# Kernel optimization log

Measured on AMD Instinct MI355X. Metric: run time of the kernel, lower is better.

## Reference

```python
import jax, jax.numpy as jnp
import numpy as np

B, S, E = 8, 2048, 768
U = 1024          # cfc_units (total NCP units; motor neurons = first E)
BB = 512          # CfC backbone width
H_MLP = 4 * E

def _lecun_tanh(x):
    return 1.7159 * jnp.tanh(0.666 * x)

def _layernorm(x, g, b, eps=1e-5):
    mu = jnp.mean(x, axis=-1, keepdims=True)
    var = jnp.var(x, axis=-1, keepdims=True)
    return (x - mu) * jax.lax.rsqrt(var + eps) * g + b


def setup_inputs() -> dict:
    key = jax.random.key(0)
    ks = jax.random.split(key, 16)
    sc = 0.02
    d = {}
    d["x"] = jax.random.normal(ks[0], (B, S, E), dtype=jnp.float32)
    d["hx"] = jnp.zeros((B, U), dtype=jnp.float32)
    # ln_1 / ln_2
    d["ln1_g"] = jnp.ones((E,), jnp.float32); d["ln1_b"] = jnp.zeros((E,), jnp.float32)
    d["ln2_g"] = jnp.ones((E,), jnp.float32); d["ln2_b"] = jnp.zeros((E,), jnp.float32)
    # CfC cell (default mode): backbone over concat([input, h]) then ff1/ff2/time_a/time_b heads
    d["W_bb"] = sc * jax.random.normal(ks[1], (E + U, BB), jnp.float32)
    d["b_bb"] = jnp.zeros((BB,), jnp.float32)
    d["W_ff1"] = sc * jax.random.normal(ks[2], (BB, U), jnp.float32)
    d["b_ff1"] = jnp.zeros((U,), jnp.float32)
    d["W_ff2"] = sc * jax.random.normal(ks[3], (BB, U), jnp.float32)
    d["b_ff2"] = jnp.zeros((U,), jnp.float32)
    d["W_ta"] = sc * jax.random.normal(ks[4], (BB, U), jnp.float32)
    d["b_ta"] = jnp.zeros((U,), jnp.float32)
    d["W_tb"] = sc * jax.random.normal(ks[5], (BB, U), jnp.float32)
    d["b_tb"] = jnp.zeros((U,), jnp.float32)
    # LIF gate params (per n_embd unit)
    d["lif_thr"] = jnp.full((E,), 0.01, jnp.float32)
    d["lif_leak"] = jnp.full((E,), 2.0, jnp.float32)
    d["lif_steep"] = jnp.full((E,), 2.0, jnp.float32)
    # MLP
    d["W1"] = sc * jax.random.normal(ks[6], (E, H_MLP), jnp.float32)
    d["b1"] = jnp.zeros((H_MLP,), jnp.float32)
    d["W2"] = sc * jax.random.normal(ks[7], (H_MLP, E), jnp.float32)
    d["b2"] = jnp.zeros((E,), jnp.float32)
    return d


def _cfc_scan(normed, hx, W_bb, b_bb, W_ff1, b_ff1, W_ff2, b_ff2, W_ta, b_ta, W_tb, b_tb):
    # normed: [B, S, E]; hx: [B, U]. Closed-form continuous-time cell, ts=1.
    xs = jnp.swapaxes(normed, 0, 1)  # [S, B, E]

    def step(h, x_t):
        cat = jnp.concatenate([x_t, h], axis=-1)           # [B, E+U]
        bb = _lecun_tanh(cat @ W_bb + b_bb)                # [B, BB]
        ff1 = _lecun_tanh(bb @ W_ff1 + b_ff1)              # [B, U]
        ff2 = _lecun_tanh(bb @ W_ff2 + b_ff2)
        t_interp = jax.nn.sigmoid((bb @ W_ta + b_ta) + (bb @ W_tb + b_tb))
        h_new = ff1 * (1.0 - t_interp) + t_interp * ff2    # [B, U]
        return h_new, h_new[:, :E]                         # motor neurons -> output

    new_hx, ys = jax.lax.scan(step, hx, xs)
    return jnp.swapaxes(ys, 0, 1), new_hx                  # [B, S, E], [B, U]


def _lif_gate(x, thr, leak, steep):
    threshold = jnp.abs(thr) * 0.1
    leak_s = jax.nn.sigmoid(leak)
    steepness = jax.nn.softplus(steep)
    potential = jnp.abs(x)
    fire = jax.nn.sigmoid(steepness * (potential - threshold))
    gate = fire + leak_s * (1.0 - fire)
    return x * gate


def reference(x, hx, ln1_g, ln1_b, ln2_g, ln2_b,
              W_bb, b_bb, W_ff1, b_ff1, W_ff2, b_ff2, W_ta, b_ta, W_tb, b_tb,
              lif_thr, lif_leak, lif_steep, W1, b1, W2, b2):
    normed = _layernorm(x, ln1_g, ln1_b)
    cfc_out, new_hx = _cfc_scan(normed, hx, W_bb, b_bb, W_ff1, b_ff1,
                                W_ff2, b_ff2, W_ta, b_ta, W_tb, b_tb)
    cfc_out = _lif_gate(cfc_out, lif_thr, lif_leak, lif_steep)
    x = x + cfc_out  # dropout = identity in eval
    h2 = _layernorm(x, ln2_g, ln2_b)
    mlp = jax.nn.gelu(h2 @ W1 + b1, approximate=False) @ W2 + b2
    x = x + mlp
    return x, new_hx
```

## Files before the change

kernel.cpp:

```cpp
#include <hip/hip_runtime.h>
#include <math.h>

#define NB 8
#define NS 2048
#define NE 768
#define NU 1024
#define NBB 512
#define NH 3072
#define NBS (NB*NS)
#define NWG 128

typedef float f32x4v __attribute__((ext_vector_type(4)));
typedef __bf16 bf16x8v __attribute__((ext_vector_type(8)));
typedef unsigned short u16x8v __attribute__((ext_vector_type(8)));
typedef unsigned short u16x4v __attribute__((ext_vector_type(4)));

__device__ __forceinline__ unsigned short f2bf(float f) {
  unsigned int u = __builtin_bit_cast(unsigned int, f);
  u = (u + 0x7fffu + ((u >> 16) & 1u)) >> 16;
  return (unsigned short)u;
}
__device__ __forceinline__ float bf2f(unsigned short h) {
  unsigned int u = ((unsigned int)h) << 16;
  return __builtin_bit_cast(float, u);
}

__device__ __forceinline__ float ald(const float* p) {
  return __hip_atomic_load((const float*)p, __ATOMIC_RELAXED, __HIP_MEMORY_SCOPE_AGENT);
}
__device__ __forceinline__ void ast(float* p, float v) {
  __hip_atomic_store(p, v, __ATOMIC_RELAXED, __HIP_MEMORY_SCOPE_AGENT);
}
__device__ __forceinline__ float2 ald2(const float* p) {
  unsigned long long v = __hip_atomic_load((const unsigned long long*)p,
                             __ATOMIC_RELAXED, __HIP_MEMORY_SCOPE_AGENT);
  return __builtin_bit_cast(float2, v);
}
__device__ __forceinline__ unsigned aldu(const unsigned* p) {
  return __hip_atomic_load(p, __ATOMIC_RELAXED, __HIP_MEMORY_SCOPE_AGENT);
}
__device__ __forceinline__ void astu(unsigned* p, unsigned v) {
  __hip_atomic_store(p, v, __ATOMIC_RELAXED, __HIP_MEMORY_SCOPE_AGENT);
}

__device__ __forceinline__ void gbar4(unsigned* bar, int bx, unsigned tick) {
  __syncthreads();
  int tid = threadIdx.x;
  unsigned* flag = &bar[768];
  if (bx == 0) {
    if (tid < 64) {
      if (tid == 0) astu(&bar[0], tick);
      unsigned m;
      do {
        unsigned a = aldu(&bar[tid * 4]);
        unsigned b = aldu(&bar[(tid + 64) * 4]);
        m = a < b ? a : b;
        #pragma unroll
        for (int s = 1; s < 64; s <<= 1) {
          unsigned o = __shfl_xor(m, s);
          m = m < o ? m : o;
        }
        if (m < tick) __builtin_amdgcn_s_sleep(1);
      } while (m < tick);
      if (tid == 0) astu(flag, tick);
    }
  } else {
    if (tid == 0) {
      astu(&bar[bx * 4], tick);
      while (aldu(flag) < tick) __builtin_amdgcn_s_sleep(1);
    }
  }
  __syncthreads();
}

__global__ __launch_bounds__(256) void tr_f32(const float* __restrict__ in,
                                              float* __restrict__ out, int R, int C) {
  __shared__ float tile[32][33];
  int c0 = blockIdx.x * 32, r0 = blockIdx.y * 32;
  int tx = threadIdx.x, ty = threadIdx.y;
  #pragma unroll
  for (int i = 0; i < 32; i += 8)
    tile[ty + i][tx] = in[(long)(r0 + ty + i) * C + c0 + tx];
  __syncthreads();
  #pragma unroll
  for (int i = 0; i < 32; i += 8)
    out[(long)(c0 + ty + i) * R + r0 + tx] = tile[tx][ty + i];
}

__global__ __launch_bounds__(256) void tr_f32_bf16(const float* __restrict__ in,
                                                   unsigned short* __restrict__ out, int R, int C) {
  __shared__ float tile[32][33];
  int c0 = blockIdx.x * 32, r0 = blockIdx.y * 32;
  int tx = threadIdx.x, ty = threadIdx.y;
  #pragma unroll
  for (int i = 0; i < 32; i += 8)
    tile[ty + i][tx] = in[(long)(r0 + ty + i) * C + c0 + tx];
  __syncthreads();
  #pragma unroll
  for (int i = 0; i < 32; i += 8)
    out[(long)(c0 + ty + i) * R + r0 + tx] = f2bf(tile[tx][ty + i]);
}

__global__ __launch_bounds__(256) void tr_f32_bf16split(const float* __restrict__ in,
    unsigned short* __restrict__ oh, unsigned short* __restrict__ ol, int R, int C) {
  __shared__ float tile[32][33];
  int c0 = blockIdx.x * 32, r0 = blockIdx.y * 32;
  int tx = threadIdx.x, ty = threadIdx.y;
  #pragma unroll
  for (int i = 0; i < 32; i += 8)
    tile[ty + i][tx] = in[(long)(r0 + ty + i) * C + c0 + tx];
  __syncthreads();
  #pragma unroll
  for (int i = 0; i < 32; i += 8) {
    float v = tile[tx][ty + i];
    unsigned short h = f2bf(v);
    long idx = (long)(c0 + ty + i) * R + r0 + tx;
    oh[idx] = h;
    ol[idx] = f2bf(v - bf2f(h));
  }
}

__global__ __launch_bounds__(256) void ln_kernel(const float* __restrict__ in,
    const float* __restrict__ gw, const float* __restrict__ bw,
    unsigned short* __restrict__ outh, unsigned short* __restrict__ outl) {
  int lane = threadIdx.x & 63;
  long row = (long)blockIdx.x * 4 + (threadIdx.x >> 6);
  const float4* rp = (const float4*)(in + row * NE);
  float4 v[3];
  float s = 0.f, sq = 0.f;
  #pragma unroll
  for (int j = 0; j < 3; ++j) {
    v[j] = rp[lane + j * 64];
    s += v[j].x + v[j].y + v[j].z + v[j].w;
    sq += v[j].x*v[j].x + v[j].y*v[j].y + v[j].z*v[j].z + v[j].w*v[j].w;
  }
  #pragma unroll
  for (int m = 1; m < 64; m <<= 1) { s += __shfl_xor(s, m); sq += __shfl_xor(sq, m); }
  float mu = s * (1.f / NE);
  float rs = rsqrtf(sq * (1.f / NE) - mu * mu + 1e-5f);
  #pragma unroll
  for (int j = 0; j < 3; ++j) {
    int c4 = lane + j * 64;
    float4 g4 = ((const float4*)gw)[c4];
    float4 b4 = ((const float4*)bw)[c4];
    float f0 = (v[j].x - mu) * rs * g4.x + b4.x;
    float f1 = (v[j].y - mu) * rs * g4.y + b4.y;
    float f2 = (v[j].z - mu) * rs * g4.z + b4.z;
    float f3 = (v[j].w - mu) * rs * g4.w + b4.w;
    u16x4v oh, ol;
    oh[0] = f2bf(f0); ol[0] = f2bf(f0 - bf2f(oh[0]));
    oh[1] = f2bf(f1); ol[1] = f2bf(f1 - bf2f(oh[1]));
    oh[2] = f2bf(f2); ol[2] = f2bf(f2 - bf2f(oh[2]));
    oh[3] = f2bf(f3); ol[3] = f2bf(f3 - bf2f(oh[3]));
    *(u16x4v*)(outh + row * NE + (long)c4 * 4) = oh;
    *(u16x4v*)(outl + row * NE + (long)c4 * 4) = ol;
  }
}

template<int EPI>
__global__ __launch_bounds__(256) void gemm_bf16(
    const unsigned short* __restrict__ A, const unsigned short* __restrict__ Bt,
    const float* __restrict__ bias, const float* res,
    float* Cf, unsigned short* Cb, int M, int N, int K)
{
  __shared__ unsigned short lA[128][72];
  __shared__ unsigned short lB[128][72];
  int tid = threadIdx.x;
  int lane = tid & 63, wave = tid >> 6;
  int wr = wave >> 1, wc = wave & 1;
  int r15 = lane & 15, hi = lane >> 4;
  int ntn = N >> 7;
  long m0 = (long)(blockIdx.x / ntn) << 7;
  long n0 = (long)(blockIdx.x % ntn) << 7;
  f32x4v acc[4][4];
  #pragma unroll
  for (int m = 0; m < 4; ++m)
    #pragma unroll
    for (int n = 0; n < 4; ++n) acc[m][n] = (f32x4v){0.f, 0.f, 0.f, 0.f};

  for (int kt = 0; kt < K; kt += 64) {
    u16x8v ra[4], rb[4];
    #pragma unroll
    for (int i = 0; i < 4; ++i) {
      int c = tid + (i << 8);
      int rw = c >> 3, ko = (c & 7) << 3;
      ra[i] = *(const u16x8v*)(A + (m0 + rw) * K + kt + ko);
      rb[i] = *(const u16x8v*)(Bt + (n0 + rw) * K + kt + ko);
    }
    __syncthreads();
    #pragma unroll
    for (int i = 0; i < 4; ++i) {
      int c = tid + (i << 8);
      int rw = c >> 3, ko = (c & 7) << 3;
      *(u16x8v*)(&lA[rw][ko]) = ra[i];
      *(u16x8v*)(&lB[rw][ko]) = rb[i];
    }
    __syncthreads();
    #pragma unroll
    for (int ks = 0; ks < 64; ks += 32) {
      bf16x8v af[4], bfr[4];
      #pragma unroll
      for (int m = 0; m < 4; ++m)
        af[m] = *(const bf16x8v*)(&lA[wr * 64 + m * 16 + r15][ks + hi * 8]);
      #pragma unroll
      for (int n = 0; n < 4; ++n)
        bfr[n] = *(const bf16x8v*)(&lB[wc * 64 + n * 16 + r15][ks + hi * 8]);
      #pragma unroll
      for (int m = 0; m < 4; ++m)
        #pragma unroll
        for (int n = 0; n < 4; ++n)
          acc[m][n] = __builtin_amdgcn_mfma_f32_16x16x32_bf16(af[m], bfr[n], acc[m][n], 0, 0, 0);
    }
  }
  #pragma unroll
  for (int m = 0; m < 4; ++m) {
    long rbase = m0 + wr * 64 + m * 16 + hi * 4;
    #pragma unroll
    for (int n = 0; n < 4; ++n) {
      long cg = n0 + wc * 64 + n * 16 + r15;
      float bs = (EPI == 3) ? 0.f : bias[cg];
      #pragma unroll
      for (int e = 0; e < 4; ++e) {
        long row = rbase + e;
        float vv = acc[m][n][e] + bs;
        if (EPI == 0) {
          Cf[row * N + cg] = vv;
        } else if (EPI == 1) {
          float gl = 0.5f * vv * (1.f + erff(vv * 0.70710678118f));
          Cb[row * N + cg] = f2bf(gl);
        } else if (EPI == 2) {
          Cf[row * N + cg] = vv + res[row * N + cg];
        } else {
          Cf[row * N + cg] += vv;
        }
      }
    }
  }
}

__global__ __launch_bounds__(256) void scan_kernel(
    const float* __restrict__ pre, const float* __restrict__ WhhT,
    const float* __restrict__ WhT,
    const float* __restrict__ bf1, const float* __restrict__ bf2,
    const float* __restrict__ bta, const float* __restrict__ btb,
    const float* __restrict__ hx,
    float* hbuf, float* bbf, float* __restrict__ cfc, unsigned* bar)
{
  __shared__ float lsd[NB * NU];
  __shared__ float lpart[4][4][2][8];
  int tid = threadIdx.x;
  int lane = tid & 63, wave = tid >> 6;
  int bx = blockIdx.x;
  int j1 = (bx << 2) + wave;
  int head = lane >> 4, v2 = (lane >> 3) & 1, jsub = lane & 7;
  int vg = (bx << 3) + (wave << 1) + v2;
  const float4* W14 = (const float4*)(WhhT + (long)j1 * NU);
  const float4* W24 = (const float4*)(WhT + ((long)head * NU + vg) * NBB);
  const float4* ls4 = (const float4*)lsd;
  float2* ls2 = (float2*)lsd;
  unsigned tick = 0;

  float4 wreg[4];
  #pragma unroll
  for (int c = 0; c < 4; ++c) wreg[c] = W14[(c << 6) + lane];
  float4 w2reg[16];
  #pragma unroll
  for (int c = 0; c < 16; ++c) w2reg[c] = W24[(c << 3) + jsub];

  int vl = tid >> 3, bq = tid & 7;
  int wv = vl >> 1, qq = vl & 1;
  int vo = (bx << 3) + vl;
  float cb1 = 0.f, cb2 = 0.f, cbt = 0.f;
  if (tid < 64) { cb1 = bf1[vo]; cb2 = bf2[vo]; cbt = bta[vo] + btb[vo]; }

  if (tid < 64) ast(&hbuf[(bx << 6) + tid], hx[(bx << 6) + tid]);

  float prv[8];
  if (lane == 0) {
    #pragma unroll
    for (int b = 0; b < 8; ++b) prv[b] = pre[((long)b * NS) * NBB + j1];
  }
  gbar4(bar, bx, ++tick);

  for (int t = 0; t < NS; ++t) {
    {
      float2 rv[16];
      #pragma unroll
      for (int i = 0; i < 16; ++i) rv[i] = ald2(&hbuf[(((i << 8) + tid) << 1)]);
      #pragma unroll
      for (int i = 0; i < 16; ++i) ls2[(i << 8) + tid] = rv[i];
    }
    __syncthreads();

    float a1[8];
    #pragma unroll
    for (int b = 0; b < 8; ++b) a1[b] = 0.f;
    #pragma unroll
    for (int c = 0; c < 4; ++c) {
      int idx = (c << 6) + lane;
      float4 w = wreg[c];
      #pragma unroll
      for (int b = 0; b < 8; ++b) {
        float4 hv = ls4[(b << 8) + idx];
        a1[b] += w.x * hv.x + w.y * hv.y + w.z * hv.z + w.w * hv.w;
      }
    }
    #pragma unroll
    for (int m = 1; m < 64; m <<= 1)
      #pragma unroll
      for (int b = 0; b < 8; ++b) a1[b] += __shfl_xor(a1[b], m);
    if (lane == 0) {
      #pragma unroll
      for (int b = 0; b < 8; ++b) {
        float s = a1[b] + prv[b];
        ast(&bbf[b * NBB + j1], 1.7159f * tanhf(0.666f * s));
      }
    }
    gbar4(bar, bx, ++tick);

    {
      float2 rv[8];
      #pragma unroll
      for (int i = 0; i < 8; ++i) rv[i] = ald2(&bbf[(((i << 8) + tid) << 1)]);
      #pragma unroll
      for (int i = 0; i < 8; ++i) ls2[(i << 8) + tid] = rv[i];
    }
    __syncthreads();

    float a2[8];
    #pragma unroll
    for (int b = 0; b < 8; ++b) a2[b] = 0.f;
    #pragma unroll
    for (int c = 0; c < 16; ++c) {
      int idx = (c << 3) + jsub;
      float4 w = w2reg[c];
      #pragma unroll
      for (int b = 0; b < 8; ++b) {
        float4 bv = ls4[(b << 7) + idx];
        a2[b] += w.x * bv.x + w.y * bv.y + w.z * bv.z + w.w * bv.w;
      }
    }
    #pragma unroll
    for (int m = 1; m < 8; m <<= 1)
      #pragma unroll
      for (int b = 0; b < 8; ++b) a2[b] += __shfl_xor(a2[b], m);
    if (jsub == 0) {
      #pragma unroll
      for (int b = 0; b < 8; ++b) lpart[wave][head][v2][b] = a2[b];
    }
    __syncthreads();
    if (tid < 64) {
      float d1 = lpart[wv][0][qq][bq] + cb1;
      float d2 = lpart[wv][1][qq][bq] + cb2;
      float dt = lpart[wv][2][qq][bq] + lpart[wv][3][qq][bq] + cbt;
      float f1 = 1.7159f * tanhf(0.666f * d1);
      float f2 = 1.7159f * tanhf(0.666f * d2);
      float ti = 1.f / (1.f + expf(-dt));
      float hn = f1 * (1.f - ti) + ti * f2;
      ast(&hbuf[bq * NU + vo], hn);
      if (vo < NE) cfc[((long)bq * NS + t) * NE + vo] = hn;
    }
    if (lane == 0 && t + 1 < NS) {
      #pragma unroll
      for (int b = 0; b < 8; ++b) prv[b] = pre[((long)b * NS + t + 1) * NBB + j1];
    }
    gbar4(bar, bx, ++tick);
  }
}

__global__ __launch_bounds__(256) void lif_kernel(
    const float* __restrict__ x, const float* __restrict__ cfc,
    const float* __restrict__ thr, const float* __restrict__ leak,
    const float* __restrict__ steep, const float* __restrict__ hbuf,
    float* __restrict__ x1, float* __restrict__ outTail)
{
  long i4 = (long)blockIdx.x * blockDim.x + threadIdx.x;
  float4 xv = ((const float4*)x)[i4];
  float4 cv = ((const float4*)cfc)[i4];
  int col = (int)((i4 << 2) % NE);
  float4 tv = *(const float4*)(thr + col);
  float4 lv = *(const float4*)(leak + col);
  float4 sv = *(const float4*)(steep + col);
  float4 r;
#define LIF1(comp) { \
    float th = fabsf(tv.comp) * 0.1f; \
    float ls = 1.f / (1.f + expf(-lv.comp)); \
    float sp = (sv.comp > 20.f) ? sv.comp : log1pf(expf(sv.comp)); \
    float fire = 1.f / (1.f + expf(-sp * (fabsf(cv.comp) - th))); \
    float gate = fire + ls * (1.f - fire); \
    r.comp = xv.comp + cv.comp * gate; }
  LIF1(x) LIF1(y) LIF1(z) LIF1(w)
#undef LIF1
  ((float4*)x1)[i4] = r;
  if (i4 < (NB * NU / 4)) {
    const float* hp = hbuf + (i4 << 2);
    float4 hv; hv.x = ald(hp); hv.y = ald(hp + 1); hv.z = ald(hp + 2); hv.w = ald(hp + 3);
    ((float4*)outTail)[i4] = hv;
  }
}

extern "C" void kernel_launch(void* const* d_in, const int* in_sizes, int n_in,
                              void* d_out, int out_size, void* d_ws, size_t ws_size,
                              hipStream_t stream) {
  (void)in_sizes; (void)n_in; (void)out_size; (void)ws_size;
  const float* x     = (const float*)d_in[0];
  const float* hx    = (const float*)d_in[1];
  const float* ln1g  = (const float*)d_in[2];
  const float* ln1b  = (const float*)d_in[3];
  const float* ln2g  = (const float*)d_in[4];
  const float* ln2b  = (const float*)d_in[5];
  const float* Wbb   = (const float*)d_in[6];
  const float* bbb   = (const float*)d_in[7];
  const float* Wff1  = (const float*)d_in[8];
  const float* bff1  = (const float*)d_in[9];
  const float* Wff2  = (const float*)d_in[10];
  const float* bff2  = (const float*)d_in[11];
  const float* Wta   = (const float*)d_in[12];
  const float* btaP  = (const float*)d_in[13];
  const float* Wtb   = (const float*)d_in[14];
  const float* btbP  = (const float*)d_in[15];
  const float* lthr  = (const float*)d_in[16];
  const float* lleak = (const float*)d_in[17];
  const float* lstp  = (const float*)d_in[18];
  const float* W1    = (const float*)d_in[19];
  const float* b1    = (const float*)d_in[20];
  const float* W2    = (const float*)d_in[21];
  const float* b2    = (const float*)d_in[22];

  char* base = (char*)d_ws;
  unsigned short* normedH = (unsigned short*)base;
  float* pre   = (float*)(base + 25165824);
  float* cfc   = (float*)(base + 58720256);
  unsigned short* gelu = (unsigned short*)base;
  unsigned short* normedL = (unsigned short*)(base + 109051904);
  unsigned short* h2      = (unsigned short*)(base + 109051904);
  unsigned short* wtbbH = (unsigned short*)(base + 134217728);
  float* whhT  = (float*)(base + 135004160);
  float* whT   = (float*)(base + 137101312);
  unsigned short* w1t = (unsigned short*)(base + 145489920);
  unsigned short* w2t = (unsigned short*)(base + 150208512);
  float* hbuf  = (float*)(base + 154927104);
  float* bbf   = (float*)(base + 154959872);
  unsigned* bar = (unsigned*)(base + 154976256);
  unsigned short* wtbbL = (unsigned short*)(base + 154980352);
  float* xout  = (float*)d_out;
  float* outTail = xout + (size_t)NBS * NE;
  unsigned short* lnlo_dummy = (unsigned short*)base;

  dim3 b328(32, 8);
  tr_f32_bf16split<<<dim3(512/32, 768/32), b328, 0, stream>>>(Wbb, wtbbH, wtbbL, 768, 512);
  tr_f32<<<dim3(512/32, 1024/32), b328, 0, stream>>>(Wbb + 768*512, whhT, 1024, 512);
  tr_f32<<<dim3(1024/32, 512/32), b328, 0, stream>>>(Wff1, whT + 0*(size_t)NU*NBB, 512, 1024);
  tr_f32<<<dim3(1024/32, 512/32), b328, 0, stream>>>(Wff2, whT + 1*(size_t)NU*NBB, 512, 1024);
  tr_f32<<<dim3(1024/32, 512/32), b328, 0, stream>>>(Wta,  whT + 2*(size_t)NU*NBB, 512, 1024);
  tr_f32<<<dim3(1024/32, 512/32), b328, 0, stream>>>(Wtb,  whT + 3*(size_t)NU*NBB, 512, 1024);
  tr_f32_bf16<<<dim3(3072/32, 768/32), b328, 0, stream>>>(W1, w1t, 768, 3072);
  tr_f32_bf16<<<dim3(768/32, 3072/32), b328, 0, stream>>>(W2, w2t, 3072, 768);

  ln_kernel<<<NBS/4, 256, 0, stream>>>(x, ln1g, ln1b, normedH, normedL);
  gemm_bf16<0><<<(NBS/128)*(NBB/128), 256, 0, stream>>>(normedH, wtbbH, bbb, nullptr,
                                                        pre, nullptr, NBS, NBB, NE);
  gemm_bf16<3><<<(NBS/128)*(NBB/128), 256, 0, stream>>>(normedH, wtbbL, bbb, nullptr,
                                                        pre, nullptr, NBS, NBB, NE);
  gemm_bf16<3><<<(NBS/128)*(NBB/128), 256, 0, stream>>>(normedL, wtbbH, bbb, nullptr,
                                                        pre, nullptr, NBS, NBB, NE);

  hipMemsetAsync(bar, 0, 4096, stream);

  scan_kernel<<<NWG, 256, 0, stream>>>(pre, whhT, whT, bff1, bff2, btaP, btbP, hx,
                                       hbuf, bbf, cfc, bar);

  lif_kernel<<<(NBS*NE/4)/256, 256, 0, stream>>>(x, cfc, lthr, lleak, lstp, hbuf, xout, outTail);
  ln_kernel<<<NBS/4, 256, 0, stream>>>(xout, ln2g, ln2b, h2, lnlo_dummy);
  gemm_bf16<1><<<(NBS/128)*(NH/128), 256, 0, stream>>>(h2, w1t, b1, nullptr,
                                                       nullptr, gelu, NBS, NH, NE);
  gemm_bf16<2><<<(NBS/128)*(NE/128), 256, 0, stream>>>(gelu, w2t, b2, xout,
                                                       xout, nullptr, NBS, NE, NH);
}
```

Measured before the change: 21.56 ms.

## Redesign scan grid barrier with per-block release flags and batched pre loads

The grid barrier now pads arrival slots to 64 bytes and gives each block its own release flag, which block 0 writes directly. The s_sleep backoff is removed so waiters spin tightly. The per-step global load of the precomputed backbone input is replaced by loading 64 timesteps into LDS at once, and the cfc output store is moved after the barrier so it is off the critical path. Together these aim to shorten the sequential scan's per-step latency. The cost is heavier spinning traffic and the barrier buffer moving to a new workspace region.

```diff
diff --git a/kernel.cpp b/kernel.cpp
--- a/kernel.cpp
+++ b/kernel.cpp
@@ -43,31 +43,30 @@
   __hip_atomic_store(p, v, __ATOMIC_RELAXED, __HIP_MEMORY_SCOPE_AGENT);
 }
 
-__device__ __forceinline__ void gbar4(unsigned* bar, int bx, unsigned tick) {
+__device__ __forceinline__ void gbar5(unsigned* bar, int bx, unsigned tick) {
   __syncthreads();
   int tid = threadIdx.x;
-  unsigned* flag = &bar[768];
   if (bx == 0) {
     if (tid < 64) {
       if (tid == 0) astu(&bar[0], tick);
       unsigned m;
       do {
-        unsigned a = aldu(&bar[tid * 4]);
-        unsigned b = aldu(&bar[(tid + 64) * 4]);
+        unsigned a = aldu(&bar[tid * 16]);
+        unsigned b = aldu(&bar[(tid + 64) * 16]);
         m = a < b ? a : b;
         #pragma unroll
         for (int s = 1; s < 64; s <<= 1) {
           unsigned o = __shfl_xor(m, s);
           m = m < o ? m : o;
         }
-        if (m < tick) __builtin_amdgcn_s_sleep(1);
       } while (m < tick);
-      if (tid == 0) astu(flag, tick);
+      astu(&bar[2048 + tid * 16], tick);
+      astu(&bar[2048 + (tid + 64) * 16], tick);
     }
   } else {
     if (tid == 0) {
-      astu(&bar[bx * 4], tick);
-      while (aldu(flag) < tick) __builtin_amdgcn_s_sleep(1);
+      astu(&bar[bx * 16], tick);
+      while (aldu(&bar[2048 + bx * 16]) < tick) {}
     }
   }
   __syncthreads();
@@ -247,6 +246,7 @@
     float* hbuf, float* bbf, float* __restrict__ cfc, unsigned* bar)
 {
   __shared__ float lsd[NB * NU];
+  __shared__ float4 lpre[512];
   __shared__ float lpart[4][4][2][8];
   int tid = threadIdx.x;
   int lane = tid & 63, wave = tid >> 6;
@@ -258,6 +258,7 @@
   const float4* W24 = (const float4*)(WhT + ((long)head * NU + vg) * NBB);
   const float4* ls4 = (const float4*)lsd;
   float2* ls2 = (float2*)lsd;
+  const float* lpf = (const float*)lpre;
   unsigned tick = 0;
 
   float4 wreg[4];
@@ -274,15 +275,17 @@
   if (tid < 64) { cb1 = bf1[vo]; cb2 = bf2[vo]; cbt = bta[vo] + btb[vo]; }
 
   if (tid < 64) ast(&hbuf[(bx << 6) + tid], hx[(bx << 6) + tid]);
-
-  float prv[8];
-  if (lane == 0) {
-    #pragma unroll
-    for (int b = 0; b < 8; ++b) prv[b] = pre[((long)b * NS) * NBB + j1];
-  }
-  gbar4(bar, bx, ++tick);
+  gbar5(bar, bx, ++tick);
 
   for (int t = 0; t < NS; ++t) {
+    if ((t & 63) == 0) {
+      #pragma unroll
+      for (int i = 0; i < 2; ++i) {
+        int idx = (i << 8) + tid;
+        int b = idx >> 6, tq = idx & 63;
+        lpre[idx] = *(const float4*)(pre + ((long)b * NS + t + tq) * NBB + (bx << 2));
+      }
+    }
     {
       float2 rv[16];
       #pragma unroll
@@ -310,13 +313,14 @@
       #pragma unroll
       for (int b = 0; b < 8; ++b) a1[b] += __shfl_xor(a1[b], m);
     if (lane == 0) {
+      int tq = t & 63;
       #pragma unroll
       for (int b = 0; b < 8; ++b) {
-        float s = a1[b] + prv[b];
+        float s = a1[b] + lpf[(((b << 6) | tq) << 2) + wave];
         ast(&bbf[b * NBB + j1], 1.7159f * tanhf(0.666f * s));
       }
     }
-    gbar4(bar, bx, ++tick);
+    gbar5(bar, bx, ++tick);
 
     {
       float2 rv[8];
@@ -349,6 +353,7 @@
       for (int b = 0; b < 8; ++b) lpart[wave][head][v2][b] = a2[b];
     }
     __syncthreads();
+    float hn = 0.f;
     if (tid < 64) {
       float d1 = lpart[wv][0][qq][bq] + cb1;
       float d2 = lpart[wv][1][qq][bq] + cb2;
@@ -356,15 +361,11 @@
       float f1 = 1.7159f * tanhf(0.666f * d1);
       float f2 = 1.7159f * tanhf(0.666f * d2);
       float ti = 1.f / (1.f + expf(-dt));
-      float hn = f1 * (1.f - ti) + ti * f2;
+      hn = f1 * (1.f - ti) + ti * f2;
       ast(&hbuf[bq * NU + vo], hn);
-      if (vo < NE) cfc[((long)bq * NS + t) * NE + vo] = hn;
-    }
-    if (lane == 0 && t + 1 < NS) {
-      #pragma unroll
-      for (int b = 0; b < 8; ++b) prv[b] = pre[((long)b * NS + t + 1) * NBB + j1];
-    }
-    gbar4(bar, bx, ++tick);
+    }
+    gbar5(bar, bx, ++tick);
+    if (tid < 64 && vo < NE) cfc[((long)bq * NS + t) * NE + vo] = hn;
   }
 }
 
@@ -434,6 +435,7 @@
   unsigned short* gelu = (unsigned short*)base;
   unsigned short* normedL = (unsigned short*)(base + 109051904);
   unsigned short* h2      = (unsigned short*)(base + 109051904);
+  unsigned* bar = (unsigned*)(base + 125829120);
   unsigned short* wtbbH = (unsigned short*)(base + 134217728);
   float* whhT  = (float*)(base + 135004160);
   float* whT   = (float*)(base + 137101312);
@@ -441,7 +443,6 @@
   unsigned short* w2t = (unsigned short*)(base + 150208512);
   float* hbuf  = (float*)(base + 154927104);
   float* bbf   = (float*)(base + 154959872);
-  unsigned* bar = (unsigned*)(base + 154976256);
   unsigned short* wtbbL = (unsigned short*)(base + 154980352);
   float* xout  = (float*)d_out;
   float* outTail = xout + (size_t)NBS * NE;
@@ -465,7 +466,7 @@
   gemm_bf16<3><<<(NBS/128)*(NBB/128), 256, 0, stream>>>(normedL, wtbbH, bbb, nullptr,
                                                         pre, nullptr, NBS, NBB, NE);
 
-  hipMemsetAsync(bar, 0, 4096, stream);
+  hipMemsetAsync(bar, 0, 16384, stream);
 
   scan_kernel<<<NWG, 256, 0, stream>>>(pre, whhT, whT, bff1, bff2, btaP, btbP, hx,
                                        hbuf, bbf, cfc, bar);
```

Result: slower. 22.59 ms (+4.7%).
